# Performance work log

Hardware: AMD Instinct MI355X
Metric: run time of the kernel (lower is better)

## Reference

```python
import jax, jax.numpy as jnp
import numpy as np

B, S, D = 4, 2048, 1024


def setup_inputs() -> dict:
    key = jax.random.key(0)
    k1, k2, k3, k4, k5 = jax.random.split(key, 5)
    x = jax.random.normal(k1, (B, S, D), dtype=jnp.float32)
    mask = jax.random.randint(k2, (B, S), 0, 2).astype(jnp.bool_)
    # glorot-uniform-like init as keras add_weight default
    lim = float(np.sqrt(6.0 / (D + D)))
    q_w = jax.random.uniform(k3, (D, D), minval=-lim, maxval=lim, dtype=jnp.float32)
    k_w = jax.random.uniform(k4, (D, D), minval=-lim, maxval=lim, dtype=jnp.float32)
    v_w = jax.random.uniform(k5, (D, D), minval=-lim, maxval=lim, dtype=jnp.float32)
    return {"x": x, "mask": mask, "q_w": q_w, "k_w": k_w, "v_w": v_w}


def reference(x, mask, q_w, k_w, v_w):
    scale = 1.0 / jnp.sqrt(jnp.asarray(x.shape[-1], dtype=x.dtype))
    q = jnp.einsum('bsi,ij->bsj', x, q_w)
    k = jnp.einsum('bsi,ij->bsj', x, k_w)
    y = jnp.einsum('bsi,bzi->bsz', q, k) * scale  # [B,S,S] scores
    # additive mask applied along the query axis, exactly as the source
    m = (~mask).astype(x.dtype)[:, :, None]
    y = y + m * (-1e9)
    v = jnp.einsum('bsi,ij->bsj', x, v_w)
    p = jax.nn.softmax(y, axis=-1)
    return jnp.einsum('bsz,bzi->bsi', p, v)
```

## Files before the change

kernel.cpp:

```cpp
#include <hip/hip_runtime.h>
#include <hip/hip_bf16.h>

typedef __attribute__((ext_vector_type(8))) short short8;
typedef __attribute__((ext_vector_type(4))) float floatx4;

struct ushort4v { unsigned short x, y, z, w; };

static __device__ __forceinline__ unsigned short f2bf(float f) {
    __hip_bfloat16 h = __float2bfloat16(f);
    return *reinterpret_cast<unsigned short*>(&h);
}

static __device__ __forceinline__ float bf2f(unsigned short u) {
    unsigned int v = ((unsigned int)u) << 16;
    return *reinterpret_cast<float*>(&v);
}

#define ASYNC_COPY16(gsrc, ldst)                                                            \
    __builtin_amdgcn_global_load_lds((const __attribute__((address_space(1))) void*)(gsrc), \
                                     (__attribute__((address_space(3))) void*)(ldst), 16, 0, 0)

static __device__ __forceinline__ void block_barrier() {
    asm volatile("" ::: "memory");
    __builtin_amdgcn_s_barrier();
    asm volatile("" ::: "memory");
}

__global__ __launch_bounds__(256) void mask_expand_fused(const unsigned char* __restrict__ m,
                                                         float* __restrict__ keep, int n) {
    __shared__ int s_or;
    if (threadIdx.x == 0) s_or = 0;
    __syncthreads();
    int acc = 0;
    for (int i = threadIdx.x; i < 8192; i += 256)
        if (i & 3) acc |= m[i];
    atomicOr(&s_or, acc);
    __syncthreads();
    const bool u8enc = (s_or != 0);
    int i = blockIdx.x * 256 + threadIdx.x;
    if (i < n) {
        bool on = u8enc ? (m[i] != 0) : (((const int*)m)[i] != 0);
        keep[i] = on ? 1.0f : 0.0f;
    }
}

__global__ __launch_bounds__(256) void convert_f32_bf16(const float* __restrict__ in,
                                                        unsigned short* __restrict__ out, long n4) {
    long i = (long)blockIdx.x * 256 + threadIdx.x;
    if (i >= n4) return;
    float4 v = ((const float4*)in)[i];
    ushort4v o;
    o.x = f2bf(v.x); o.y = f2bf(v.y); o.z = f2bf(v.z); o.w = f2bf(v.w);
    ((ushort4v*)out)[i] = o;
}

__global__ void transpose_w_kernel(const float* __restrict__ w0, const float* __restrict__ w1,
                                   const float* __restrict__ w2, unsigned short* __restrict__ out) {
    __shared__ float t[32][33];
    const float* w = blockIdx.z == 0 ? w0 : (blockIdx.z == 1 ? w1 : w2);
    unsigned short* o = out + (long)blockIdx.z * 1024 * 1024;
    int c0 = blockIdx.x * 32, r0 = blockIdx.y * 32;
    for (int i = threadIdx.y; i < 32; i += 8)
        t[i][threadIdx.x] = w[(long)(r0 + i) * 1024 + c0 + threadIdx.x];
    __syncthreads();
    for (int i = threadIdx.y; i < 32; i += 8)
        o[(long)(c0 + i) * 1024 + r0 + threadIdx.x] = f2bf(t[threadIdx.x][i]);
}

template <int EPI>
static __device__ __forceinline__ void gemm8_body(const unsigned short* __restrict__ A,
                                                  const unsigned short* __restrict__ B,
                                                  void* __restrict__ Cv,
                                                  unsigned short* __restrict__ vt,
                                                  const float* __restrict__ aux,
                                                  int K, int lda, int ldb, int ldc,
                                                  long sA, long sB, long sC, long sAux,
                                                  float scale) {
    constexpr int TILE = (128 + 256) * 32 * 2;
    __shared__ char sm[3 * TILE];

    const int tid = threadIdx.x;
    const int wid = tid >> 6, lane = tid & 63;
    const int wm  = wid >> 2, wn = wid & 3;
    const int fr  = lane & 15, fk = lane >> 4;
    const long m0 = (long)blockIdx.x * 128;
    const long n0 = (long)blockIdx.y * 256;
    const unsigned short* Ab = A + (long)blockIdx.z * sA + m0 * lda;
    const unsigned short* Bb = B + (long)blockIdx.z * sB + n0 * ldb;
    const int NT = K >> 5;

    floatx4 acc[4][4] = {};

    auto stage = [&](int kt, int buf) {
        char* dA = sm + buf * TILE;
        char* dB = dA + 128 * 64;
        const int kb = kt << 5;
        {
            int lam = tid * 16;
            int lg  = lam ^ (((lam >> 7) & 3) << 4);
            ASYNC_COPY16(Ab + (long)(lg >> 6) * lda + kb + ((lg & 63) >> 1), dA + lam);
        }
#pragma unroll
        for (int i = 0; i < 2; i++) {
            int lam = i * 8192 + tid * 16;
            int lg  = lam ^ (((lam >> 7) & 3) << 4);
            ASYNC_COPY16(Bb + (long)(lg >> 6) * ldb + kb + ((lg & 63) >> 1), dB + lam);
        }
    };

    stage(0, 0);
    stage(1, 1);

    int cur = 0;
    for (int t = 0; t < NT; t++) {
        if (t + 1 < NT) asm volatile("s_waitcnt vmcnt(3)" ::: "memory");
        else            asm volatile("s_waitcnt vmcnt(0)" ::: "memory");
        block_barrier();

        const char* bA = sm + cur * TILE;
        const char* bB = bA + 128 * 64;
        short8 af[4], bf[4];
#pragma unroll
        for (int mi = 0; mi < 4; mi++) {
            int row = wm * 64 + mi * 16 + fr;
            int c   = (fk * 16) ^ (((row >> 1) & 3) << 4);
            af[mi] = *(const short8*)(bA + row * 64 + c);
        }
#pragma unroll
        for (int ni = 0; ni < 4; ni++) {
            int row = wn * 64 + ni * 16 + fr;
            int c   = (fk * 16) ^ (((row >> 1) & 3) << 4);
            bf[ni] = *(const short8*)(bB + row * 64 + c);
        }
        if (t + 2 < NT) stage(t + 2, (cur + 2) % 3);

        __builtin_amdgcn_s_setprio(1);
#pragma unroll
        for (int mi = 0; mi < 4; mi++)
#pragma unroll
            for (int ni = 0; ni < 4; ni++)
                acc[mi][ni] = __builtin_amdgcn_mfma_f32_16x16x32_bf16(af[mi], bf[ni], acc[mi][ni], 0, 0, 0);
        __builtin_amdgcn_s_setprio(0);
        cur = (cur == 2) ? 0 : cur + 1;
    }

    const int crow = (lane >> 4) * 4;
    const int ccol = lane & 15;

    if (EPI == 0 && blockIdx.z == 2) {
        block_barrier();
        unsigned short* T = (unsigned short*)sm;
        constexpr int LDT = 132;
#pragma unroll
        for (int mi = 0; mi < 4; mi++)
#pragma unroll
            for (int j = 0; j < 4; j++) {
                int rl = wm * 64 + mi * 16 + crow + j;
#pragma unroll
                for (int ni = 0; ni < 4; ni++) {
                    int cl = wn * 64 + ni * 16 + ccol;
                    T[cl * LDT + rl] = f2bf(acc[mi][ni][j]);
                }
            }
        block_barrier();
        const long bb   = m0 >> 11;
        const long sloc = m0 & 2047;
        unsigned short* vb = vt + bb * (1024L * 2048) + sloc;
#pragma unroll
        for (int p = 0; p < 8; p++) {
            int chunk = p * 512 + tid;
            int d  = chunk >> 4;
            int s0 = (chunk & 15) * 8;
            short8 v = *(const short8*)&T[d * LDT + s0];
            *(short8*)(vb + (n0 + d) * 2048 + s0) = v;
        }
        return;
    }

#pragma unroll
    for (int mi = 0; mi < 4; mi++) {
#pragma unroll
        for (int j = 0; j < 4; j++) {
            long r = m0 + wm * 64 + mi * 16 + crow + j;
            float rowf = 0.0f;
            if (EPI == 1) rowf = scale * aux[(long)blockIdx.z * sAux + r];
            if (EPI == 2) rowf = aux[(long)blockIdx.z * sAux + r];
#pragma unroll
            for (int ni = 0; ni < 4; ni++) {
                long c = n0 + wn * 64 + ni * 16 + ccol;
                float v = acc[mi][ni][j];
                if (EPI == 0) {
                    ((unsigned short*)Cv)[(long)blockIdx.z * sC + r * ldc + c] = f2bf(v);
                } else if (EPI == 1) {
                    ((unsigned short*)Cv)[(long)blockIdx.z * sC + r * ldc + c] = f2bf(__expf(v * rowf));
                } else {
                    ((float*)Cv)[(long)blockIdx.z * sC + r * ldc + c] = v * rowf;
                }
            }
        }
    }
}

__global__ __launch_bounds__(512, 4) void gemm8_qkv(const unsigned short* __restrict__ A,
                                                    const unsigned short* __restrict__ B,
                                                    void* __restrict__ Cv,
                                                    unsigned short* __restrict__ vt,
                                                    int K, int lda, int ldb, int ldc,
                                                    long sA, long sB, long sC) {
    gemm8_body<0>(A, B, Cv, vt, nullptr, K, lda, ldb, ldc, sA, sB, sC, 0L, 1.0f);
}

__global__ __launch_bounds__(512, 4) void gemm8_scores(const unsigned short* __restrict__ A,
                                                       const unsigned short* __restrict__ B,
                                                       void* __restrict__ Cv,
                                                       const float* __restrict__ keep,
                                                       int K, int lda, int ldb, int ldc,
                                                       long sA, long sB, long sC, long sAux,
                                                       float scale) {
    gemm8_body<1>(A, B, Cv, nullptr, keep, K, lda, ldb, ldc, sA, sB, sC, sAux, scale);
}

__global__ __launch_bounds__(512, 4) void gemm8_pv(const unsigned short* __restrict__ A,
                                                   const unsigned short* __restrict__ B,
                                                   void* __restrict__ Cv,
                                                   const float* __restrict__ invsum,
                                                   int K, int lda, int ldb, int ldc,
                                                   long sA, long sB, long sC, long sAux) {
    gemm8_body<2>(A, B, Cv, nullptr, invsum, K, lda, ldb, ldc, sA, sB, sC, sAux, 1.0f);
}

__global__ __launch_bounds__(256) void rowsum_inv(const unsigned short* __restrict__ P,
                                                  float* __restrict__ inv, long strideP) {
    const int tid = threadIdx.x;
    const long row = blockIdx.x;
    short8 v = ((const short8*)(P + row * strideP))[tid];
    float s = 0.0f;
#pragma unroll
    for (int i = 0; i < 8; i++) s += bf2f((unsigned short)v[i]);
#pragma unroll
    for (int i = 1; i < 64; i <<= 1) s += __shfl_xor(s, i);
    __shared__ float ss[4];
    if ((tid & 63) == 0) ss[tid >> 6] = s;
    __syncthreads();
    if (tid == 0) {
        float t = (ss[0] + ss[1]) + (ss[2] + ss[3]);
        inv[row] = 1.0f / t;
    }
}

extern "C" void kernel_launch(void* const* d_in, const int* in_sizes, int n_in,
                              void* d_out, int out_size, void* d_ws, size_t ws_size,
                              hipStream_t stream) {
    const float* x  = (const float*)d_in[0];
    const void*  mask = d_in[1];
    const float* qw = (const float*)d_in[2];
    const float* kw = (const float*)d_in[3];
    const float* vw = (const float*)d_in[4];
    float* out = (float*)d_out;

    constexpr int B = 4, S = 2048, D = 1024;
    constexpr long BS  = (long)B * S;
    constexpr long BSD = BS * D;

    char* w = (char*)d_ws;
    auto alloc = [&](size_t bytes) {
        char* p = w;
        w += (bytes + 255) & ~(size_t)255;
        return p;
    };
    float*          keep    = (float*)alloc(BS * 4);
    float*          invsum  = (float*)alloc(BS * 4);
    unsigned short* xb      = (unsigned short*)alloc((size_t)BSD * 2);
    unsigned short* wT      = (unsigned short*)alloc((size_t)3 * D * D * 2);
    unsigned short* qk      = (unsigned short*)alloc((size_t)2 * BSD * 2);
    unsigned short* Qb = qk;
    unsigned short* Kb = qk + BSD;
    unsigned short* Vt      = (unsigned short*)alloc((size_t)BSD * 2);

    size_t base_used = (size_t)(w - (char*)d_ws);
    size_t pB = (size_t)B * S * S * 2;
    bool batched = ws_size >= base_used + pB + 1024;

    unsigned short* P;
    if (batched) {
        P = (unsigned short*)alloc(pB);
    } else {
        P = (unsigned short*)alloc((size_t)S * S * 2);
    }

    const float scale = 0.03125f;

    mask_expand_fused<<<(int)(BS / 256), 256, 0, stream>>>((const unsigned char*)mask, keep, (int)BS);
    convert_f32_bf16<<<(int)(BSD / 1024), 256, 0, stream>>>(x, xb, BSD / 4);
    transpose_w_kernel<<<dim3(32, 32, 3), dim3(32, 8), 0, stream>>>(qw, kw, vw, wT);

    gemm8_qkv<<<dim3(64, 4, 3), 512, 0, stream>>>(xb, wT, qk, Vt,
                                                  1024, 1024, 1024, 1024,
                                                  0L, (long)D * D, BSD);

    if (batched) {
        gemm8_scores<<<dim3(16, 8, B), 512, 0, stream>>>(Qb, Kb, P, keep,
                                                         1024, 1024, 1024, 2048,
                                                         (long)S * D, (long)S * D, (long)S * S, (long)S, scale);
        rowsum_inv<<<(int)BS, 256, 0, stream>>>(P, invsum, 2048);
        gemm8_pv<<<dim3(16, 4, B), 512, 0, stream>>>(P, Vt, out, invsum,
                                                     2048, 2048, 2048, 1024,
                                                     (long)S * S, (long)D * S, (long)S * D, (long)S);
    } else {
        for (int b = 0; b < B; b++) {
            gemm8_scores<<<dim3(16, 8, 1), 512, 0, stream>>>(Qb + (long)b * S * D, Kb + (long)b * S * D,
                                                             P, keep + (long)b * S,
                                                             1024, 1024, 1024, 2048,
                                                             0L, 0L, 0L, 0L, scale);
            rowsum_inv<<<S, 256, 0, stream>>>(P, invsum + (long)b * S, 2048);
            gemm8_pv<<<dim3(16, 4, 1), 512, 0, stream>>>(P, Vt + (long)b * D * S, out + (long)b * S * D,
                                                         invsum + (long)b * S,
                                                         2048, 2048, 2048, 1024,
                                                         0L, 0L, 0L, 0L);
        }
    }
}
```

Measured before the change: 171.4 us.

## Fuse softmax row-sum into PV GEMM by summing A fragments in registers

Removes the separate rowsum_inv kernel, which reread the full bf16 probability matrix. Instead, the wn==0 waves of the PV GEMM accumulate the bf16 P fragments they already load from LDS, reduce them across lanes and pass them through shared memory. The epilogue then divides each output row by its sum. This saves a kernel launch and a full pass over P, but adds ALU work and an extra barrier to one quarter of the waves in the main loop.

```diff
diff --git a/kernel.cpp b/kernel.cpp
--- a/kernel.cpp
+++ b/kernel.cpp
@@ -90,6 +90,7 @@
     const int NT = K >> 5;
 
     floatx4 acc[4][4] = {};
+    float rsum[4] = {0.f, 0.f, 0.f, 0.f};
 
     auto stage = [&](int kt, int buf) {
         char* dA = sm + buf * TILE;
@@ -134,6 +135,14 @@
         }
         if (t + 2 < NT) stage(t + 2, (cur + 2) % 3);
 
+        if (EPI == 2 && wn == 0) {
+#pragma unroll
+            for (int mi = 0; mi < 4; mi++)
+#pragma unroll
+                for (int j = 0; j < 8; j++)
+                    rsum[mi] += bf2f((unsigned short)af[mi][j]);
+        }
+
         __builtin_amdgcn_s_setprio(1);
 #pragma unroll
         for (int mi = 0; mi < 4; mi++)
@@ -177,6 +186,21 @@
         return;
     }
 
+    float* rs = (float*)sm;
+    if (EPI == 2) {
+        block_barrier();
+        if (wn == 0) {
+#pragma unroll
+            for (int mi = 0; mi < 4; mi++) {
+                float s = rsum[mi];
+                s += __shfl_xor(s, 16);
+                s += __shfl_xor(s, 32);
+                if ((lane >> 4) == 0) rs[wm * 64 + mi * 16 + fr] = s;
+            }
+        }
+        block_barrier();
+    }
+
 #pragma unroll
     for (int mi = 0; mi < 4; mi++) {
 #pragma unroll
@@ -184,7 +208,7 @@
             long r = m0 + wm * 64 + mi * 16 + crow + j;
             float rowf = 0.0f;
             if (EPI == 1) rowf = scale * aux[(long)blockIdx.z * sAux + r];
-            if (EPI == 2) rowf = aux[(long)blockIdx.z * sAux + r];
+            if (EPI == 2) rowf = 1.0f / rs[wm * 64 + mi * 16 + crow + j];
 #pragma unroll
             for (int ni = 0; ni < 4; ni++) {
                 long c = n0 + wn * 64 + ni * 16 + ccol;
@@ -223,29 +247,9 @@
 __global__ __launch_bounds__(512, 4) void gemm8_pv(const unsigned short* __restrict__ A,
                                                    const unsigned short* __restrict__ B,
                                                    void* __restrict__ Cv,
-                                                   const float* __restrict__ invsum,
                                                    int K, int lda, int ldb, int ldc,
-                                                   long sA, long sB, long sC, long sAux) {
-    gemm8_body<2>(A, B, Cv, nullptr, invsum, K, lda, ldb, ldc, sA, sB, sC, sAux, 1.0f);
-}
-
-__global__ __launch_bounds__(256) void rowsum_inv(const unsigned short* __restrict__ P,
-                                                  float* __restrict__ inv, long strideP) {
-    const int tid = threadIdx.x;
-    const long row = blockIdx.x;
-    short8 v = ((const short8*)(P + row * strideP))[tid];
-    float s = 0.0f;
-#pragma unroll
-    for (int i = 0; i < 8; i++) s += bf2f((unsigned short)v[i]);
-#pragma unroll
-    for (int i = 1; i < 64; i <<= 1) s += __shfl_xor(s, i);
-    __shared__ float ss[4];
-    if ((tid & 63) == 0) ss[tid >> 6] = s;
-    __syncthreads();
-    if (tid == 0) {
-        float t = (ss[0] + ss[1]) + (ss[2] + ss[3]);
-        inv[row] = 1.0f / t;
-    }
+                                                   long sA, long sB, long sC) {
+    gemm8_body<2>(A, B, Cv, nullptr, nullptr, K, lda, ldb, ldc, sA, sB, sC, 0L, 1.0f);
 }
 
 extern "C" void kernel_launch(void* const* d_in, const int* in_sizes, int n_in,
@@ -269,7 +273,6 @@
         return p;
     };
     float*          keep    = (float*)alloc(BS * 4);
-    float*          invsum  = (float*)alloc(BS * 4);
     unsigned short* xb      = (unsigned short*)alloc((size_t)BSD * 2);
     unsigned short* wT      = (unsigned short*)alloc((size_t)3 * D * D * 2);
     unsigned short* qk      = (unsigned short*)alloc((size_t)2 * BSD * 2);
@@ -302,21 +305,18 @@
         gemm8_scores<<<dim3(16, 8, B), 512, 0, stream>>>(Qb, Kb, P, keep,
                                                          1024, 1024, 1024, 2048,
                                                          (long)S * D, (long)S * D, (long)S * S, (long)S, scale);
-        rowsum_inv<<<(int)BS, 256, 0, stream>>>(P, invsum, 2048);
-        gemm8_pv<<<dim3(16, 4, B), 512, 0, stream>>>(P, Vt, out, invsum,
+        gemm8_pv<<<dim3(16, 4, B), 512, 0, stream>>>(P, Vt, out,
                                                      2048, 2048, 2048, 1024,
-                                                     (long)S * S, (long)D * S, (long)S * D, (long)S);
+                                                     (long)S * S, (long)D * S, (long)S * D);
     } else {
         for (int b = 0; b < B; b++) {
             gemm8_scores<<<dim3(16, 8, 1), 512, 0, stream>>>(Qb + (long)b * S * D, Kb + (long)b * S * D,
                                                              P, keep + (long)b * S,
                                                              1024, 1024, 1024, 2048,
                                                              0L, 0L, 0L, 0L, scale);
-            rowsum_inv<<<S, 256, 0, stream>>>(P, invsum + (long)b * S, 2048);
             gemm8_pv<<<dim3(16, 4, 1), 512, 0, stream>>>(P, Vt + (long)b * D * S, out + (long)b * S * D,
-                                                         invsum + (long)b * S,
                                                          2048, 2048, 2048, 1024,
-                                                         0L, 0L, 0L, 0L);
-        }
-    }
-}
+                                                         0L, 0L, 0L);
+        }
+    }
+}
```

Measured after the change: 172.7 us. No clear change (+0.8%).

## Fuse prep kernels and double-buffer QKV GEMM to raise occupancy

Applied to the files above, without the earlier changes.

Merges the mask expansion, x-to-bf16 conversion and weight transpose into one launch that dispatches on block index, which removes two kernel launches. The QKV GEMM moves from triple to double buffering so it uses less shared memory, and its launch bounds rise from 4 to 6 waves per SIMD so more blocks can be resident. Because the smaller buffer can no longer hold the whole 128x256 V tile, the V-transpose epilogue now writes it out in two halves. The cost is less latency hiding per block: each step waits for all loads with vmcnt(0), and the tighter launch bound may cap registers and cause spills.

```diff
diff --git a/kernel.cpp b/kernel.cpp
--- a/kernel.cpp
+++ b/kernel.cpp
@@ -26,48 +26,56 @@
     asm volatile("" ::: "memory");
 }
 
-__global__ __launch_bounds__(256) void mask_expand_fused(const unsigned char* __restrict__ m,
-                                                         float* __restrict__ keep, int n) {
+__global__ __launch_bounds__(256) void prep_kernel(const float* __restrict__ x,
+                                                   unsigned short* __restrict__ xb,
+                                                   const float* __restrict__ w0,
+                                                   const float* __restrict__ w1,
+                                                   const float* __restrict__ w2,
+                                                   unsigned short* __restrict__ wT,
+                                                   const unsigned char* __restrict__ mask,
+                                                   float* __restrict__ keep, int nMask) {
+    __shared__ float t[32][33];
     __shared__ int s_or;
-    if (threadIdx.x == 0) s_or = 0;
-    __syncthreads();
-    int acc = 0;
-    for (int i = threadIdx.x; i < 8192; i += 256)
-        if (i & 3) acc |= m[i];
-    atomicOr(&s_or, acc);
-    __syncthreads();
-    const bool u8enc = (s_or != 0);
-    int i = blockIdx.x * 256 + threadIdx.x;
-    if (i < n) {
-        bool on = u8enc ? (m[i] != 0) : (((const int*)m)[i] != 0);
-        keep[i] = on ? 1.0f : 0.0f;
-    }
-}
-
-__global__ __launch_bounds__(256) void convert_f32_bf16(const float* __restrict__ in,
-                                                        unsigned short* __restrict__ out, long n4) {
-    long i = (long)blockIdx.x * 256 + threadIdx.x;
-    if (i >= n4) return;
-    float4 v = ((const float4*)in)[i];
-    ushort4v o;
-    o.x = f2bf(v.x); o.y = f2bf(v.y); o.z = f2bf(v.z); o.w = f2bf(v.w);
-    ((ushort4v*)out)[i] = o;
-}
-
-__global__ void transpose_w_kernel(const float* __restrict__ w0, const float* __restrict__ w1,
-                                   const float* __restrict__ w2, unsigned short* __restrict__ out) {
-    __shared__ float t[32][33];
-    const float* w = blockIdx.z == 0 ? w0 : (blockIdx.z == 1 ? w1 : w2);
-    unsigned short* o = out + (long)blockIdx.z * 1024 * 1024;
-    int c0 = blockIdx.x * 32, r0 = blockIdx.y * 32;
-    for (int i = threadIdx.y; i < 32; i += 8)
-        t[i][threadIdx.x] = w[(long)(r0 + i) * 1024 + c0 + threadIdx.x];
-    __syncthreads();
-    for (int i = threadIdx.y; i < 32; i += 8)
-        o[(long)(c0 + i) * 1024 + r0 + threadIdx.x] = f2bf(t[threadIdx.x][i]);
-}
-
-template <int EPI>
+    const int b = blockIdx.x;
+    const int tid = threadIdx.x;
+
+    if (b < 8192) {
+        long i = (long)b * 256 + tid;
+        float4 v = ((const float4*)x)[i];
+        ushort4v o;
+        o.x = f2bf(v.x); o.y = f2bf(v.y); o.z = f2bf(v.z); o.w = f2bf(v.w);
+        ((ushort4v*)xb)[i] = o;
+    } else if (b < 11264) {
+        int idx = b - 8192;
+        int z = idx >> 10, rem = idx & 1023;
+        int bx = rem & 31, by = rem >> 5;
+        const float* w = z == 0 ? w0 : (z == 1 ? w1 : w2);
+        unsigned short* o = wT + (long)z * 1024 * 1024;
+        int c0 = bx * 32, r0 = by * 32;
+        int tx = tid & 31, ty = tid >> 5;
+        for (int i = ty; i < 32; i += 8)
+            t[i][tx] = w[(long)(r0 + i) * 1024 + c0 + tx];
+        __syncthreads();
+        for (int i = ty; i < 32; i += 8)
+            o[(long)(c0 + i) * 1024 + r0 + tx] = f2bf(t[tx][i]);
+    } else {
+        if (tid == 0) s_or = 0;
+        __syncthreads();
+        int acc = 0;
+        for (int i = tid; i < 8192; i += 256)
+            if (i & 3) acc |= mask[i];
+        atomicOr(&s_or, acc);
+        __syncthreads();
+        const bool u8enc = (s_or != 0);
+        int i = (b - 11264) * 256 + tid;
+        if (i < nMask) {
+            bool on = u8enc ? (mask[i] != 0) : (((const int*)mask)[i] != 0);
+            keep[i] = on ? 1.0f : 0.0f;
+        }
+    }
+}
+
+template <int EPI, int DEPTH>
 static __device__ __forceinline__ void gemm8_body(const unsigned short* __restrict__ A,
                                                   const unsigned short* __restrict__ B,
                                                   void* __restrict__ Cv,
@@ -77,7 +85,7 @@
                                                   long sA, long sB, long sC, long sAux,
                                                   float scale) {
     constexpr int TILE = (128 + 256) * 32 * 2;
-    __shared__ char sm[3 * TILE];
+    __shared__ char sm[DEPTH * TILE];
 
     const int tid = threadIdx.x;
     const int wid = tid >> 6, lane = tid & 63;
@@ -109,12 +117,16 @@
     };
 
     stage(0, 0);
-    stage(1, 1);
+    if (DEPTH == 3) stage(1, 1);
 
     int cur = 0;
     for (int t = 0; t < NT; t++) {
-        if (t + 1 < NT) asm volatile("s_waitcnt vmcnt(3)" ::: "memory");
-        else            asm volatile("s_waitcnt vmcnt(0)" ::: "memory");
+        if (DEPTH == 3) {
+            if (t + 1 < NT) asm volatile("s_waitcnt vmcnt(3)" ::: "memory");
+            else            asm volatile("s_waitcnt vmcnt(0)" ::: "memory");
+        } else {
+            asm volatile("s_waitcnt vmcnt(0)" ::: "memory");
+        }
         block_barrier();
 
         const char* bA = sm + cur * TILE;
@@ -132,7 +144,11 @@
             int c   = (fk * 16) ^ (((row >> 1) & 3) << 4);
             bf[ni] = *(const short8*)(bB + row * 64 + c);
         }
-        if (t + 2 < NT) stage(t + 2, (cur + 2) % 3);
+        if (DEPTH == 3) {
+            if (t + 2 < NT) stage(t + 2, (cur + 2) % 3);
+        } else {
+            if (t + 1 < NT) stage(t + 1, cur ^ 1);
+        }
 
         __builtin_amdgcn_s_setprio(1);
 #pragma unroll
@@ -141,38 +157,43 @@
             for (int ni = 0; ni < 4; ni++)
                 acc[mi][ni] = __builtin_amdgcn_mfma_f32_16x16x32_bf16(af[mi], bf[ni], acc[mi][ni], 0, 0, 0);
         __builtin_amdgcn_s_setprio(0);
-        cur = (cur == 2) ? 0 : cur + 1;
+        cur = (DEPTH == 3) ? ((cur == 2) ? 0 : cur + 1) : (cur ^ 1);
     }
 
     const int crow = (lane >> 4) * 4;
     const int ccol = lane & 15;
 
     if (EPI == 0 && blockIdx.z == 2) {
-        block_barrier();
         unsigned short* T = (unsigned short*)sm;
         constexpr int LDT = 132;
-#pragma unroll
-        for (int mi = 0; mi < 4; mi++)
-#pragma unroll
-            for (int j = 0; j < 4; j++) {
-                int rl = wm * 64 + mi * 16 + crow + j;
-#pragma unroll
-                for (int ni = 0; ni < 4; ni++) {
-                    int cl = wn * 64 + ni * 16 + ccol;
-                    T[cl * LDT + rl] = f2bf(acc[mi][ni][j]);
-                }
-            }
-        block_barrier();
         const long bb   = m0 >> 11;
         const long sloc = m0 & 2047;
         unsigned short* vb = vt + bb * (1024L * 2048) + sloc;
 #pragma unroll
-        for (int p = 0; p < 8; p++) {
-            int chunk = p * 512 + tid;
-            int d  = chunk >> 4;
-            int s0 = (chunk & 15) * 8;
-            short8 v = *(const short8*)&T[d * LDT + s0];
-            *(short8*)(vb + (n0 + d) * 2048 + s0) = v;
+        for (int dh = 0; dh < 2; dh++) {
+            block_barrier();
+            if ((wn >> 1) == dh) {
+#pragma unroll
+                for (int mi = 0; mi < 4; mi++)
+#pragma unroll
+                    for (int j = 0; j < 4; j++) {
+                        int rl = wm * 64 + mi * 16 + crow + j;
+#pragma unroll
+                        for (int ni = 0; ni < 4; ni++) {
+                            int clh = (wn & 1) * 64 + ni * 16 + ccol;
+                            T[clh * LDT + rl] = f2bf(acc[mi][ni][j]);
+                        }
+                    }
+            }
+            block_barrier();
+#pragma unroll
+            for (int p = 0; p < 4; p++) {
+                int chunk = p * 512 + tid;
+                int d  = chunk >> 4;
+                int s0 = (chunk & 15) * 8;
+                short8 v = *(const short8*)&T[d * LDT + s0];
+                *(short8*)(vb + (n0 + dh * 128 + d) * 2048 + s0) = v;
+            }
         }
         return;
     }
@@ -201,13 +222,13 @@
     }
 }
 
-__global__ __launch_bounds__(512, 4) void gemm8_qkv(const unsigned short* __restrict__ A,
+__global__ __launch_bounds__(512, 6) void gemm8_qkv(const unsigned short* __restrict__ A,
                                                     const unsigned short* __restrict__ B,
                                                     void* __restrict__ Cv,
                                                     unsigned short* __restrict__ vt,
                                                     int K, int lda, int ldb, int ldc,
                                                     long sA, long sB, long sC) {
-    gemm8_body<0>(A, B, Cv, vt, nullptr, K, lda, ldb, ldc, sA, sB, sC, 0L, 1.0f);
+    gemm8_body<0, 2>(A, B, Cv, vt, nullptr, K, lda, ldb, ldc, sA, sB, sC, 0L, 1.0f);
 }
 
 __global__ __launch_bounds__(512, 4) void gemm8_scores(const unsigned short* __restrict__ A,
@@ -217,7 +238,7 @@
                                                        int K, int lda, int ldb, int ldc,
                                                        long sA, long sB, long sC, long sAux,
                                                        float scale) {
-    gemm8_body<1>(A, B, Cv, nullptr, keep, K, lda, ldb, ldc, sA, sB, sC, sAux, scale);
+    gemm8_body<1, 3>(A, B, Cv, nullptr, keep, K, lda, ldb, ldc, sA, sB, sC, sAux, scale);
 }
 
 __global__ __launch_bounds__(512, 4) void gemm8_pv(const unsigned short* __restrict__ A,
@@ -226,7 +247,7 @@
                                                    const float* __restrict__ invsum,
                                                    int K, int lda, int ldb, int ldc,
                                                    long sA, long sB, long sC, long sAux) {
-    gemm8_body<2>(A, B, Cv, nullptr, invsum, K, lda, ldb, ldc, sA, sB, sC, sAux, 1.0f);
+    gemm8_body<2, 3>(A, B, Cv, nullptr, invsum, K, lda, ldb, ldc, sA, sB, sC, sAux, 1.0f);
 }
 
 __global__ __launch_bounds__(256) void rowsum_inv(const unsigned short* __restrict__ P,
@@ -290,9 +311,8 @@
 
     const float scale = 0.03125f;
 
-    mask_expand_fused<<<(int)(BS / 256), 256, 0, stream>>>((const unsigned char*)mask, keep, (int)BS);
-    convert_f32_bf16<<<(int)(BSD / 1024), 256, 0, stream>>>(x, xb, BSD / 4);
-    transpose_w_kernel<<<dim3(32, 32, 3), dim3(32, 8), 0, stream>>>(qw, kw, vw, wT);
+    prep_kernel<<<11296, 256, 0, stream>>>(x, xb, qw, kw, vw, wT,
+                                           (const unsigned char*)mask, keep, (int)BS);
 
     gemm8_qkv<<<dim3(64, 4, 3), 512, 0, stream>>>(xb, wT, qk, Vt,
                                                   1024, 1024, 1024, 1024,
```

Result: slower. 581.1 us (+239.1%).
